# Kernel optimization log

Measured on AMD Instinct MI355X. Metric: run time of the kernel, lower is better.

## Reference

```python
import jax, jax.numpy as jnp
import numpy as np

B, C, H, W = 8, 8, 512, 512

# one-pixel shifts with zero padding (equivalent to the bmm with shift matrices)
def shift_right(x):  # out[..., c] = x[..., c-1]
    return jnp.pad(x, ((0, 0), (0, 0), (1, 0)))[:, :, :-1]
def shift_left(x):   # out[..., c] = x[..., c+1]
    return jnp.pad(x, ((0, 0), (0, 0), (0, 1)))[:, :, 1:]
def shift_up(x):     # out[r] = x[r+1]
    return jnp.pad(x, ((0, 0), (0, 1), (0, 0)))[:, 1:, :]
def shift_down(x):   # out[r] = x[r-1]
    return jnp.pad(x, ((0, 0), (1, 0), (0, 0)))[:, :-1, :]

def bilater_voting(c):
    # c: [B, 8, H, W] probabilities
    right        = shift_right(c[:, 4])
    left         = shift_left(c[:, 3])
    left_bottom  = shift_left(shift_down(c[:, 5]))
    right_above  = shift_right(shift_up(c[:, 2]))
    left_above   = shift_left(shift_up(c[:, 0]))
    bottom       = shift_down(c[:, 6])
    up           = shift_up(c[:, 1])
    right_bottom = shift_right(shift_down(c[:, 7]))
    a1 = c[:, 3] * right
    a2 = c[:, 4] * left
    a3 = c[:, 1] * bottom
    a4 = c[:, 6] * up
    a5 = c[:, 2] * left_bottom
    a6 = c[:, 5] * right_above
    a7 = c[:, 0] * right_bottom
    a8 = c[:, 7] * left_above
    vote_out = jnp.stack([a7, a3, a5, a1, a2, a6, a4, a8], axis=1)
    glo_map = jnp.mean(vote_out, axis=1)
    return glo_map, vote_out

def bce(p, t):
    # matches torch F.binary_cross_entropy (mean reduction, log clamped at -100)
    logp = jnp.clip(jnp.log(p), -100.0, None)
    log1mp = jnp.clip(jnp.log(1.0 - p), -100.0, None)
    return -jnp.mean(t * logp + (1.0 - t) * log1mp)

def setup_inputs() -> dict:
    key = jax.random.key(0)
    k1, k2, k3, k4 = jax.random.split(key, 4)
    atts = jax.random.normal(k1, (B, C, H, W), dtype=jnp.float32)
    dets = jax.random.normal(k2, (B, C, H, W), dtype=jnp.float32)
    target = jax.random.randint(k3, (B, 1, H, W), 0, 2).astype(jnp.float32)
    con_target = jax.random.randint(k4, (B, C, H, W), 0, 2).astype(jnp.float32)
    return {"atts": atts, "dets": dets, "target": target, "con_target": con_target}

def reference(atts, dets, target, con_target):
    # edge mask from connectivity GT: pixels with 0 < sum < 8
    sum_conn = jnp.sum(con_target, axis=1)  # [B, H, W]
    edge_conn = jnp.where((sum_conn < 8.0) & (sum_conn > 0.0), 1.0, 0.0)

    atts_p = jax.nn.sigmoid(atts)
    dets_p = jax.nn.sigmoid(dets)

    glo_map1, vote_out1 = bilater_voting(atts_p)
    glo_map2, vote_out2 = bilater_voting(dets_p)

    # edge/decouple loss on dets branch
    pred_mask_min = 1.0 - jnp.min(vote_out2, axis=1)
    pred_mask_min = pred_mask_min * edge_conn
    decouple_map = glo_map2 * (1.0 - edge_conn) + pred_mask_min
    de_loss2 = bce(decouple_map[:, None], target)

    bce_loss1 = bce(glo_map1[:, None], target)
    bicon_loss1 = bce(vote_out1, con_target)
    conn_loss1 = bce(atts_p, con_target)
    bicon_loss2 = bce(vote_out2, con_target)
    conn_loss2 = bce(dets_p, con_target)

    loss = (0.2 * bicon_loss1 + 0.8 * conn_loss1 + bce_loss1
            + 0.2 * bicon_loss2 + 0.8 * conn_loss2 + de_loss2)
    return loss
```

## Files before the change

kernel.cpp:

```cpp
#include <hip/hip_runtime.h>
#include <stdint.h>

#define BB 8
#define CC 8
#define HH 512
#define WW 512
#define HWSZ (HH * WW)

typedef float v4 __attribute__((ext_vector_type(4)));

#define LOG2_CLAMP -144.26950409f

__device__ __forceinline__ v4 uload4(const float* __restrict__ p) {
    v4 r;
    __builtin_memcpy(&r, p, sizeof(v4));
    return r;
}
__device__ __forceinline__ v4 aload4(const float* __restrict__ p) {
    return *(const v4* __restrict__)p;
}

__device__ __forceinline__ v4 sig4(v4 x) {
    v4 r;
#pragma unroll
    for (int i = 0; i < 4; ++i)
        r[i] = __builtin_amdgcn_rcpf(1.0f + __expf(-x[i]));
    return r;
}

template <bool NEED_MIN>
__device__ __forceinline__ void eval_branch(
    const v4* __restrict__ cr, const v4* __restrict__ nr, uint32_t sel,
    const float* __restrict__ mkA, const float* __restrict__ mkB,
    const float* __restrict__ mkC,
    v4& glo, v4& vmin, float& Lbic, float& Lcon)
{
    const v4 one = {1.f, 1.f, 1.f, 1.f};
    v4 pb0 = one, pb1 = one, pc = one;
    v4 vsum = {0.f, 0.f, 0.f, 0.f};
    if (NEED_MIN) vmin = {1e30f, 1e30f, 1e30f, 1e30f};

#pragma unroll
    for (int k = 0; k < 8; ++k) {
        v4 s = sig4(cr[k]);
        v4 n = sig4(nr[k]);
        n[0] *= mkA[k]; n[1] *= mkB[k]; n[2] *= mkB[k]; n[3] *= mkC[k];
        v4 v = s * n;
        vsum += v;
        if (NEED_MIN) vmin = __builtin_elementwise_min(vmin, v);
        v4 av, as;
#pragma unroll
        for (int i = 0; i < 4; ++i) {
            const bool bt = (sel >> (k * 4 + i)) & 1u;
            av[i] = bt ? v[i] : 1.0f - v[i];
            as[i] = bt ? s[i] : 1.0f - s[i];
        }
        if (k < 4) pb0 *= av; else pb1 *= av;
        pc *= as;
    }
    glo = vsum * 0.125f;

    float lb = 0.f, lc = 0.f;
#pragma unroll
    for (int i = 0; i < 4; ++i) {
        lb += fmaxf(__log2f(pb0[i]), LOG2_CLAMP) + fmaxf(__log2f(pb1[i]), LOG2_CLAMP);
        lc += fmaxf(__log2f(pc[i]), LOG2_CLAMP);
    }
    Lbic = lb;
    Lcon = lc;
}

__global__ __launch_bounds__(256, 2) void bicon_loss_kernel(
    const float* __restrict__ atts, const float* __restrict__ dets,
    const float* __restrict__ target, const float* __restrict__ con,
    float* __restrict__ partial)
{
    const int idx = (int)blockIdx.x * 256 + (int)threadIdx.x;
    const int w0  = (idx & 127) << 2;
    const int row = idx >> 7;
    const int h   = row & (HH - 1);
    const int b   = row >> 9;

    const int hm = (h > 0) ? h - 1 : 0;
    const int hp = (h < HH - 1) ? h + 1 : HH - 1;
    const float mh0 = (h > 0) ? 1.0f : 0.0f;
    const float mh1 = (h < HH - 1) ? 1.0f : 0.0f;
    const float mw0 = (w0 == 0) ? 0.0f : 1.0f;
    const float mw3 = (w0 == WW - 4) ? 0.0f : 1.0f;

    const int offC = h * WW + w0;
    const int offU = hm * WW + w0;
    const int offD = hp * WW + w0;

    const float* __restrict__ ab = atts + b * CC * HWSZ;
    const float* __restrict__ db = dets + b * CC * HWSZ;
    const float* __restrict__ cb = con  + b * CC * HWSZ;

    v4 cvv[8];
#pragma unroll
    for (int c = 0; c < 8; ++c) cvv[c] = aload4(cb + c * HWSZ + offC);
    v4 tv = aload4(target + b * HWSZ + offC);

    v4 ac[8], an[8];
#pragma unroll
    for (int c = 0; c < 8; ++c) ac[c] = aload4(ab + c * HWSZ + offC);
    an[0] = uload4(ab + 7 * HWSZ + offU - 1);
    an[1] = aload4(ab + 6 * HWSZ + offU);
    an[2] = uload4(ab + 5 * HWSZ + offU + 1);
    an[3] = uload4(ab + 4 * HWSZ + offC - 1);
    an[4] = uload4(ab + 3 * HWSZ + offC + 1);
    an[5] = uload4(ab + 2 * HWSZ + offD - 1);
    an[6] = aload4(ab + 1 * HWSZ + offD);
    an[7] = uload4(ab + 0 * HWSZ + offD + 1);

    v4 dc[8], dn[8];
#pragma unroll
    for (int c = 0; c < 8; ++c) dc[c] = aload4(db + c * HWSZ + offC);
    dn[0] = uload4(db + 7 * HWSZ + offU - 1);
    dn[1] = aload4(db + 6 * HWSZ + offU);
    dn[2] = uload4(db + 5 * HWSZ + offU + 1);
    dn[3] = uload4(db + 4 * HWSZ + offC - 1);
    dn[4] = uload4(db + 3 * HWSZ + offC + 1);
    dn[5] = uload4(db + 2 * HWSZ + offD - 1);
    dn[6] = aload4(db + 1 * HWSZ + offD);
    dn[7] = uload4(db + 0 * HWSZ + offD + 1);

    uint32_t sel = 0u;
#pragma unroll
    for (int c = 0; c < 8; ++c)
#pragma unroll
        for (int i = 0; i < 4; ++i)
            if (cvv[c][i] > 0.5f) sel |= (1u << (c * 4 + i));
    uint32_t tb = 0u;
#pragma unroll
    for (int i = 0; i < 4; ++i)
        if (tv[i] > 0.5f) tb |= (1u << i);

    const float mkA[8] = {mh0 * mw0, mh0, mh0,       mw0, 1.f, mh1 * mw0, mh1, mh1};
    const float mkB[8] = {mh0,       mh0, mh0,       1.f, 1.f, mh1,       mh1, mh1};
    const float mkC[8] = {mh0,       mh0, mh0 * mw3, 1.f, mw3, mh1,       mh1, mh1 * mw3};

    v4 glo1, glo2, vmin1, vmin2;
    float Lb1, Lc1, Lb2, Lc2;
    eval_branch<false>(ac, an, sel, mkA, mkB, mkC, glo1, vmin1, Lb1, Lc1);
    eval_branch<true >(dc, dn, sel, mkA, mkB, mkC, glo2, vmin2, Lb2, Lc2);

    float Lp = 0.f;
#pragma unroll
    for (int i = 0; i < 4; ++i) {
        const uint32_t mI    = 0x11111111u << i;
        const uint32_t bitsI = sel & mI;
        const bool edge = (bitsI != 0u) && (bitsI != mI);
        const float dec = edge ? (1.0f - vmin2[i]) : glo2[i];
        const bool  ti  = (tb >> i) & 1u;
        const float a   = ti ? glo1[i] : 1.0f - glo1[i];
        const float bs  = ti ? dec     : 1.0f - dec;
        Lp += fmaxf(__log2f(a * bs), LOG2_CLAMP);
    }

    const float wbic = 0.2f / (float)(BB * CC * HWSZ);
    const float wcon = 0.8f / (float)(BB * CC * HWSZ);
    const float wpix = 1.0f / (float)(BB * HWSZ);
    const float ln2  = 0.69314718056f;

    float local = -(wbic * (Lb1 + Lb2) + wcon * (Lc1 + Lc2) + wpix * Lp) * ln2;

#pragma unroll
    for (int off = 32; off > 0; off >>= 1)
        local += __shfl_down(local, off, 64);

    __shared__ float wsum[4];
    const int lane = threadIdx.x & 63;
    const int wid  = threadIdx.x >> 6;
    if (lane == 0) wsum[wid] = local;
    __syncthreads();
    if (threadIdx.x == 0)
        partial[blockIdx.x] = wsum[0] + wsum[1] + wsum[2] + wsum[3];
}

__global__ __launch_bounds__(256, 1) void reduce_kernel(
    const float* __restrict__ partial, float* __restrict__ out)
{
    const int tid = (int)threadIdx.x;
    float s = 0.f;
#pragma unroll
    for (int i = 0; i < 8; ++i) s += partial[tid + i * 256];
#pragma unroll
    for (int off = 32; off > 0; off >>= 1)
        s += __shfl_down(s, off, 64);
    __shared__ float ws[4];
    if ((tid & 63) == 0) ws[tid >> 6] = s;
    __syncthreads();
    if (tid == 0) out[0] = ws[0] + ws[1] + ws[2] + ws[3];
}

extern "C" void kernel_launch(void* const* d_in, const int* in_sizes, int n_in,
                              void* d_out, int out_size, void* d_ws, size_t ws_size,
                              hipStream_t stream) {
    const float* atts   = (const float*)d_in[0];
    const float* dets   = (const float*)d_in[1];
    const float* target = (const float*)d_in[2];
    const float* con    = (const float*)d_in[3];
    float* out     = (float*)d_out;
    float* partial = (float*)d_ws;

    const int nblocks = BB * HH * WW / 4 / 256;
    bicon_loss_kernel<<<nblocks, 256, 0, stream>>>(atts, dets, target, con, partial);
    reduce_kernel<<<1, 256, 0, stream>>>(partial, out);
}
```

Before: 202.5 us.

## Process two rows per thread and fetch horizontal neighbours via lane shuffles

Each thread now computes two adjacent rows of four pixels, so the vertical neighbour data for the inner rows comes from registers instead of extra global loads. Horizontal one-pixel shifts are built with wave shuffles of the aligned vectors instead of unaligned vector loads. Only the wave-edge lanes fall back to scalar global loads. The aim is to cut redundant and misaligned memory traffic, at the cost of roughly doubling live registers per thread, which risks spills or lower occupancy. The grid is halved and the final reduction is adjusted to match.

```diff
diff --git a/kernel.cpp b/kernel.cpp
--- a/kernel.cpp
+++ b/kernel.cpp
@@ -11,11 +11,6 @@
 
 #define LOG2_CLAMP -144.26950409f
 
-__device__ __forceinline__ v4 uload4(const float* __restrict__ p) {
-    v4 r;
-    __builtin_memcpy(&r, p, sizeof(v4));
-    return r;
-}
 __device__ __forceinline__ v4 aload4(const float* __restrict__ p) {
     return *(const v4* __restrict__)p;
 }
@@ -28,8 +23,15 @@
     return r;
 }
 
+__device__ __forceinline__ void mk_masks(float mh0, float mh1, float mw0, float mw3,
+                                         float* A, float* B, float* C) {
+    A[0]=mh0*mw0; A[1]=mh0; A[2]=mh0;     A[3]=mw0; A[4]=1.f; A[5]=mh1*mw0; A[6]=mh1; A[7]=mh1;
+    B[0]=mh0;     B[1]=mh0; B[2]=mh0;     B[3]=1.f; B[4]=1.f; B[5]=mh1;     B[6]=mh1; B[7]=mh1;
+    C[0]=mh0;     C[1]=mh0; C[2]=mh0*mw3; C[3]=1.f; C[4]=mw3; C[5]=mh1;     C[6]=mh1; C[7]=mh1*mw3;
+}
+
 template <bool NEED_MIN>
-__device__ __forceinline__ void eval_branch(
+__device__ __forceinline__ void eval_row(
     const v4* __restrict__ cr, const v4* __restrict__ nr, uint32_t sel,
     const float* __restrict__ mkA, const float* __restrict__ mkB,
     const float* __restrict__ mkC,
@@ -59,15 +61,75 @@
         pc *= as;
     }
     glo = vsum * 0.125f;
-
-    float lb = 0.f, lc = 0.f;
 #pragma unroll
     for (int i = 0; i < 4; ++i) {
-        lb += fmaxf(__log2f(pb0[i]), LOG2_CLAMP) + fmaxf(__log2f(pb1[i]), LOG2_CLAMP);
-        lc += fmaxf(__log2f(pc[i]), LOG2_CLAMP);
-    }
-    Lbic = lb;
-    Lcon = lc;
+        Lbic += fmaxf(__log2f(pb0[i]), LOG2_CLAMP) + fmaxf(__log2f(pb1[i]), LOG2_CLAMP);
+        Lcon += fmaxf(__log2f(pc[i]), LOG2_CLAMP);
+    }
+}
+
+template <bool NEED_MIN>
+__device__ __forceinline__ void eval_input(
+    const float* __restrict__ Xb,
+    const v4* __restrict__ x0, const v4* __restrict__ x1,
+    v4 xu7, v4 xu6, v4 xu5, v4 xd2, v4 xd1, v4 xd0,
+    int offC0, int offC1, int offU, int offD, int lane,
+    uint32_t sel0, uint32_t sel1,
+    const float* __restrict__ mkA0, const float* __restrict__ mkB0,
+    const float* __restrict__ mkC0,
+    const float* __restrict__ mkA1, const float* __restrict__ mkB1,
+    const float* __restrict__ mkC1,
+    v4& glo0, v4& glo1, v4& vmin0, v4& vmin1, float& Lb, float& Lc)
+{
+    float cm[6] = { __shfl(xu7[3],   lane - 1, 64),
+                    __shfl(x0[4][3], lane - 1, 64),
+                    __shfl(x1[2][3], lane - 1, 64),
+                    __shfl(x0[7][3], lane - 1, 64),
+                    __shfl(x1[4][3], lane - 1, 64),
+                    __shfl(xd2[3],   lane - 1, 64) };
+    if (lane == 0) {
+        cm[0] = Xb[7 * HWSZ + offU  - 1];
+        cm[1] = Xb[4 * HWSZ + offC0 - 1];
+        cm[2] = Xb[2 * HWSZ + offC1 - 1];
+        cm[3] = Xb[7 * HWSZ + offC0 - 1];
+        cm[4] = Xb[4 * HWSZ + offC1 - 1];
+        cm[5] = Xb[2 * HWSZ + offD  - 1];
+    }
+    float cp[6] = { __shfl(xu5[0],   lane + 1, 64),
+                    __shfl(x0[3][0], lane + 1, 64),
+                    __shfl(x1[0][0], lane + 1, 64),
+                    __shfl(x0[5][0], lane + 1, 64),
+                    __shfl(x1[3][0], lane + 1, 64),
+                    __shfl(xd0[0],   lane + 1, 64) };
+    if (lane == 63) {
+        cp[0] = Xb[5 * HWSZ + offU  + 4];
+        cp[1] = Xb[3 * HWSZ + offC0 + 4];
+        cp[2] = Xb[0 * HWSZ + offC1 + 4];
+        cp[3] = Xb[5 * HWSZ + offC0 + 4];
+        cp[4] = Xb[3 * HWSZ + offC1 + 4];
+        cp[5] = Xb[0 * HWSZ + offD  + 4];
+    }
+
+    v4 n[8];
+    n[0] = (v4){cm[0], xu7[0], xu7[1], xu7[2]};
+    n[1] = xu6;
+    n[2] = (v4){xu5[1], xu5[2], xu5[3], cp[0]};
+    n[3] = (v4){cm[1], x0[4][0], x0[4][1], x0[4][2]};
+    n[4] = (v4){x0[3][1], x0[3][2], x0[3][3], cp[1]};
+    n[5] = (v4){cm[2], x1[2][0], x1[2][1], x1[2][2]};
+    n[6] = x1[1];
+    n[7] = (v4){x1[0][1], x1[0][2], x1[0][3], cp[2]};
+    eval_row<NEED_MIN>(x0, n, sel0, mkA0, mkB0, mkC0, glo0, vmin0, Lb, Lc);
+
+    n[0] = (v4){cm[3], x0[7][0], x0[7][1], x0[7][2]};
+    n[1] = x0[6];
+    n[2] = (v4){x0[5][1], x0[5][2], x0[5][3], cp[3]};
+    n[3] = (v4){cm[4], x1[4][0], x1[4][1], x1[4][2]};
+    n[4] = (v4){x1[3][1], x1[3][2], x1[3][3], cp[4]};
+    n[5] = (v4){cm[5], xd2[0], xd2[1], xd2[2]};
+    n[6] = xd1;
+    n[7] = (v4){xd0[1], xd0[2], xd0[3], cp[5]};
+    eval_row<NEED_MIN>(x1, n, sel1, mkA1, mkB1, mkC1, glo1, vmin1, Lb, Lc);
 }
 
 __global__ __launch_bounds__(256, 2) void bicon_loss_kernel(
@@ -75,87 +137,117 @@
     const float* __restrict__ target, const float* __restrict__ con,
     float* __restrict__ partial)
 {
-    const int idx = (int)blockIdx.x * 256 + (int)threadIdx.x;
-    const int w0  = (idx & 127) << 2;
-    const int row = idx >> 7;
-    const int h   = row & (HH - 1);
-    const int b   = row >> 9;
-
-    const int hm = (h > 0) ? h - 1 : 0;
-    const int hp = (h < HH - 1) ? h + 1 : HH - 1;
-    const float mh0 = (h > 0) ? 1.0f : 0.0f;
-    const float mh1 = (h < HH - 1) ? 1.0f : 0.0f;
-    const float mw0 = (w0 == 0) ? 0.0f : 1.0f;
-    const float mw3 = (w0 == WW - 4) ? 0.0f : 1.0f;
-
-    const int offC = h * WW + w0;
-    const int offU = hm * WW + w0;
-    const int offD = hp * WW + w0;
+    const int tid   = (int)threadIdx.x;
+    const int bid   = (int)blockIdx.x;
+    const int b     = bid >> 7;
+    const int br    = bid & 127;
+    const int strip = tid >> 7;
+    const int cg    = tid & 127;
+    const int lane  = tid & 63;
+    const int h     = br * 4 + strip * 2;
+    const int w0    = cg << 2;
+
+    const int hm  = (h > 0) ? h - 1 : 0;
+    const int hp2 = (h + 2 < HH) ? h + 2 : HH - 1;
+
+    const float mw0   = (w0 == 0) ? 0.f : 1.f;
+    const float mw3   = (w0 == WW - 4) ? 0.f : 1.f;
+    const float mh0r0 = (h > 0) ? 1.f : 0.f;
+    const float mh1r1 = (h + 1 < HH - 1) ? 1.f : 0.f;
+
+    const int offC0 = h * WW + w0;
+    const int offC1 = offC0 + WW;
+    const int offU  = hm * WW + w0;
+    const int offD  = hp2 * WW + w0;
 
     const float* __restrict__ ab = atts + b * CC * HWSZ;
     const float* __restrict__ db = dets + b * CC * HWSZ;
     const float* __restrict__ cb = con  + b * CC * HWSZ;
 
-    v4 cvv[8];
-#pragma unroll
-    for (int c = 0; c < 8; ++c) cvv[c] = aload4(cb + c * HWSZ + offC);
-    v4 tv = aload4(target + b * HWSZ + offC);
-
-    v4 ac[8], an[8];
-#pragma unroll
-    for (int c = 0; c < 8; ++c) ac[c] = aload4(ab + c * HWSZ + offC);
-    an[0] = uload4(ab + 7 * HWSZ + offU - 1);
-    an[1] = aload4(ab + 6 * HWSZ + offU);
-    an[2] = uload4(ab + 5 * HWSZ + offU + 1);
-    an[3] = uload4(ab + 4 * HWSZ + offC - 1);
-    an[4] = uload4(ab + 3 * HWSZ + offC + 1);
-    an[5] = uload4(ab + 2 * HWSZ + offD - 1);
-    an[6] = aload4(ab + 1 * HWSZ + offD);
-    an[7] = uload4(ab + 0 * HWSZ + offD + 1);
-
-    v4 dc[8], dn[8];
-#pragma unroll
-    for (int c = 0; c < 8; ++c) dc[c] = aload4(db + c * HWSZ + offC);
-    dn[0] = uload4(db + 7 * HWSZ + offU - 1);
-    dn[1] = aload4(db + 6 * HWSZ + offU);
-    dn[2] = uload4(db + 5 * HWSZ + offU + 1);
-    dn[3] = uload4(db + 4 * HWSZ + offC - 1);
-    dn[4] = uload4(db + 3 * HWSZ + offC + 1);
-    dn[5] = uload4(db + 2 * HWSZ + offD - 1);
-    dn[6] = aload4(db + 1 * HWSZ + offD);
-    dn[7] = uload4(db + 0 * HWSZ + offD + 1);
-
-    uint32_t sel = 0u;
+    v4 cv0[8], cv1[8];
+#pragma unroll
+    for (int c = 0; c < 8; ++c) {
+        cv0[c] = aload4(cb + c * HWSZ + offC0);
+        cv1[c] = aload4(cb + c * HWSZ + offC1);
+    }
+    v4 tv0 = aload4(target + b * HWSZ + offC0);
+    v4 tv1 = aload4(target + b * HWSZ + offC1);
+
+    v4 a0[8], a1[8];
+#pragma unroll
+    for (int c = 0; c < 8; ++c) {
+        a0[c] = aload4(ab + c * HWSZ + offC0);
+        a1[c] = aload4(ab + c * HWSZ + offC1);
+    }
+    v4 au7 = aload4(ab + 7 * HWSZ + offU);
+    v4 au6 = aload4(ab + 6 * HWSZ + offU);
+    v4 au5 = aload4(ab + 5 * HWSZ + offU);
+    v4 ad2 = aload4(ab + 2 * HWSZ + offD);
+    v4 ad1 = aload4(ab + 1 * HWSZ + offD);
+    v4 ad0 = aload4(ab + 0 * HWSZ + offD);
+
+    v4 d0[8], d1[8];
+#pragma unroll
+    for (int c = 0; c < 8; ++c) {
+        d0[c] = aload4(db + c * HWSZ + offC0);
+        d1[c] = aload4(db + c * HWSZ + offC1);
+    }
+    v4 du7 = aload4(db + 7 * HWSZ + offU);
+    v4 du6 = aload4(db + 6 * HWSZ + offU);
+    v4 du5 = aload4(db + 5 * HWSZ + offU);
+    v4 dd2 = aload4(db + 2 * HWSZ + offD);
+    v4 dd1 = aload4(db + 1 * HWSZ + offD);
+    v4 dd0 = aload4(db + 0 * HWSZ + offD);
+
+    uint32_t sel0 = 0u, sel1 = 0u;
 #pragma unroll
     for (int c = 0; c < 8; ++c)
 #pragma unroll
-        for (int i = 0; i < 4; ++i)
-            if (cvv[c][i] > 0.5f) sel |= (1u << (c * 4 + i));
-    uint32_t tb = 0u;
-#pragma unroll
-    for (int i = 0; i < 4; ++i)
-        if (tv[i] > 0.5f) tb |= (1u << i);
-
-    const float mkA[8] = {mh0 * mw0, mh0, mh0,       mw0, 1.f, mh1 * mw0, mh1, mh1};
-    const float mkB[8] = {mh0,       mh0, mh0,       1.f, 1.f, mh1,       mh1, mh1};
-    const float mkC[8] = {mh0,       mh0, mh0 * mw3, 1.f, mw3, mh1,       mh1, mh1 * mw3};
-
-    v4 glo1, glo2, vmin1, vmin2;
-    float Lb1, Lc1, Lb2, Lc2;
-    eval_branch<false>(ac, an, sel, mkA, mkB, mkC, glo1, vmin1, Lb1, Lc1);
-    eval_branch<true >(dc, dn, sel, mkA, mkB, mkC, glo2, vmin2, Lb2, Lc2);
+        for (int i = 0; i < 4; ++i) {
+            if (cv0[c][i] > 0.5f) sel0 |= (1u << (c * 4 + i));
+            if (cv1[c][i] > 0.5f) sel1 |= (1u << (c * 4 + i));
+        }
+    uint32_t tb0 = 0u, tb1 = 0u;
+#pragma unroll
+    for (int i = 0; i < 4; ++i) {
+        if (tv0[i] > 0.5f) tb0 |= (1u << i);
+        if (tv1[i] > 0.5f) tb1 |= (1u << i);
+    }
+
+    float mkA0[8], mkB0[8], mkC0[8], mkA1[8], mkB1[8], mkC1[8];
+    mk_masks(mh0r0, 1.f, mw0, mw3, mkA0, mkB0, mkC0);
+    mk_masks(1.f, mh1r1, mw0, mw3, mkA1, mkB1, mkC1);
+
+    float Lb1 = 0.f, Lc1 = 0.f, Lb2 = 0.f, Lc2 = 0.f;
+    v4 g1r0, g1r1, g2r0, g2r1, vm2r0, vm2r1, vdum0, vdum1;
+    eval_input<false>(ab, a0, a1, au7, au6, au5, ad2, ad1, ad0,
+                      offC0, offC1, offU, offD, lane, sel0, sel1,
+                      mkA0, mkB0, mkC0, mkA1, mkB1, mkC1,
+                      g1r0, g1r1, vdum0, vdum1, Lb1, Lc1);
+    eval_input<true >(db, d0, d1, du7, du6, du5, dd2, dd1, dd0,
+                      offC0, offC1, offU, offD, lane, sel0, sel1,
+                      mkA0, mkB0, mkC0, mkA1, mkB1, mkC1,
+                      g2r0, g2r1, vm2r0, vm2r1, Lb2, Lc2);
 
     float Lp = 0.f;
 #pragma unroll
-    for (int i = 0; i < 4; ++i) {
-        const uint32_t mI    = 0x11111111u << i;
-        const uint32_t bitsI = sel & mI;
-        const bool edge = (bitsI != 0u) && (bitsI != mI);
-        const float dec = edge ? (1.0f - vmin2[i]) : glo2[i];
-        const bool  ti  = (tb >> i) & 1u;
-        const float a   = ti ? glo1[i] : 1.0f - glo1[i];
-        const float bs  = ti ? dec     : 1.0f - dec;
-        Lp += fmaxf(__log2f(a * bs), LOG2_CLAMP);
+    for (int r = 0; r < 2; ++r) {
+        const uint32_t sel = r ? sel1 : sel0;
+        const uint32_t tb  = r ? tb1  : tb0;
+        const v4 g1 = r ? g1r1 : g1r0;
+        const v4 g2 = r ? g2r1 : g2r0;
+        const v4 vm = r ? vm2r1 : vm2r0;
+#pragma unroll
+        for (int i = 0; i < 4; ++i) {
+            const uint32_t mI    = 0x11111111u << i;
+            const uint32_t bitsI = sel & mI;
+            const bool edge = (bitsI != 0u) && (bitsI != mI);
+            const float dec = edge ? (1.0f - vm[i]) : g2[i];
+            const bool  ti  = (tb >> i) & 1u;
+            const float aa  = ti ? g1[i] : 1.0f - g1[i];
+            const float bs  = ti ? dec   : 1.0f - dec;
+            Lp += fmaxf(__log2f(aa * bs), LOG2_CLAMP);
+        }
     }
 
     const float wbic = 0.2f / (float)(BB * CC * HWSZ);
@@ -170,12 +262,11 @@
         local += __shfl_down(local, off, 64);
 
     __shared__ float wsum[4];
-    const int lane = threadIdx.x & 63;
-    const int wid  = threadIdx.x >> 6;
+    const int wid = tid >> 6;
     if (lane == 0) wsum[wid] = local;
     __syncthreads();
-    if (threadIdx.x == 0)
-        partial[blockIdx.x] = wsum[0] + wsum[1] + wsum[2] + wsum[3];
+    if (tid == 0)
+        partial[bid] = wsum[0] + wsum[1] + wsum[2] + wsum[3];
 }
 
 __global__ __launch_bounds__(256, 1) void reduce_kernel(
@@ -184,7 +275,7 @@
     const int tid = (int)threadIdx.x;
     float s = 0.f;
 #pragma unroll
-    for (int i = 0; i < 8; ++i) s += partial[tid + i * 256];
+    for (int i = 0; i < 4; ++i) s += partial[tid + i * 256];
 #pragma unroll
     for (int off = 32; off > 0; off >>= 1)
         s += __shfl_down(s, off, 64);
@@ -204,7 +295,7 @@
     float* out     = (float*)d_out;
     float* partial = (float*)d_ws;
 
-    const int nblocks = BB * HH * WW / 4 / 256;
+    const int nblocks = BB * (HH / 4);
     bicon_loss_kernel<<<nblocks, 256, 0, stream>>>(atts, dets, target, con, partial);
     reduce_kernel<<<1, 256, 0, stream>>>(partial, out);
 }
```

Result: slower. 243.9 us (+20.4%).

## Share stencil neighbors via wave shuffles with 2-row wave tiles

Applied to the files above, without the earlier changes.

Each wavefront now covers two adjacent rows of 128 columns. Vertical neighbors come from the paired half-wave via lane-xor-32 shuffles, and horizontal neighbors from adjacent-lane shuffles. Each thread loads only three aligned halo vectors plus a few scalar edge values, replacing eight unaligned neighbor loads per input. This cuts global load count and unaligned accesses, in exchange for many cross-lane shuffle instructions and extra register pressure.

```diff
diff --git a/kernel.cpp b/kernel.cpp
--- a/kernel.cpp
+++ b/kernel.cpp
@@ -11,11 +11,6 @@
 
 #define LOG2_CLAMP -144.26950409f
 
-__device__ __forceinline__ v4 uload4(const float* __restrict__ p) {
-    v4 r;
-    __builtin_memcpy(&r, p, sizeof(v4));
-    return r;
-}
 __device__ __forceinline__ v4 aload4(const float* __restrict__ p) {
     return *(const v4* __restrict__)p;
 }
@@ -28,11 +23,17 @@
     return r;
 }
 
+__device__ __forceinline__ v4 shflv4(v4 v, int src) {
+    v4 r;
+#pragma unroll
+    for (int i = 0; i < 4; ++i) r[i] = __shfl(v[i], src, 64);
+    return r;
+}
+
 template <bool NEED_MIN>
-__device__ __forceinline__ void eval_branch(
+__device__ __forceinline__ void eval_row(
     const v4* __restrict__ cr, const v4* __restrict__ nr, uint32_t sel,
-    const float* __restrict__ mkA, const float* __restrict__ mkB,
-    const float* __restrict__ mkC,
+    float mh0, float mh1, float mw0, float mw3,
     v4& glo, v4& vmin, float& Lbic, float& Lcon)
 {
     const v4 one = {1.f, 1.f, 1.f, 1.f};
@@ -42,9 +43,12 @@
 
 #pragma unroll
     for (int k = 0; k < 8; ++k) {
+        const float rowm = (k < 3) ? mh0 : ((k >= 5) ? mh1 : 1.f);
+        const float m0 = (k == 0 || k == 3 || k == 5) ? mw0 * rowm : rowm;
+        const float m3 = (k == 2 || k == 4 || k == 7) ? mw3 * rowm : rowm;
         v4 s = sig4(cr[k]);
         v4 n = sig4(nr[k]);
-        n[0] *= mkA[k]; n[1] *= mkB[k]; n[2] *= mkB[k]; n[3] *= mkC[k];
+        n[0] *= m0; n[1] *= rowm; n[2] *= rowm; n[3] *= m3;
         v4 v = s * n;
         vsum += v;
         if (NEED_MIN) vmin = __builtin_elementwise_min(vmin, v);
@@ -59,15 +63,50 @@
         pc *= as;
     }
     glo = vsum * 0.125f;
-
-    float lb = 0.f, lc = 0.f;
 #pragma unroll
     for (int i = 0; i < 4; ++i) {
-        lb += fmaxf(__log2f(pb0[i]), LOG2_CLAMP) + fmaxf(__log2f(pb1[i]), LOG2_CLAMP);
-        lc += fmaxf(__log2f(pc[i]), LOG2_CLAMP);
-    }
-    Lbic = lb;
-    Lcon = lc;
+        Lbic += fmaxf(__log2f(pb0[i]), LOG2_CLAMP) + fmaxf(__log2f(pb1[i]), LOG2_CLAMP);
+        Lcon += fmaxf(__log2f(pc[i]), LOG2_CLAMP);
+    }
+}
+
+template <bool NEED_MIN>
+__device__ __forceinline__ void eval_input(
+    const v4* __restrict__ x, const v4* __restrict__ hq,
+    const float* __restrict__ cL, const float* __restrict__ cR,
+    int lane, int rsel, int cg, uint32_t sel,
+    float mh0, float mh1, float mw0, float mw3,
+    v4& glo, v4& vmin, float& Lb, float& Lc)
+{
+    const int po = lane ^ 32;
+    v4 s7 = shflv4(x[7], po), s6 = shflv4(x[6], po), s5 = shflv4(x[5], po);
+    v4 s2 = shflv4(x[2], po), s1 = shflv4(x[1], po), s0 = shflv4(x[0], po);
+    const v4 up7 = rsel ? s7 : hq[0];
+    const v4 up6 = rsel ? s6 : hq[1];
+    const v4 up5 = rsel ? s5 : hq[2];
+    const v4 dn2 = rsel ? hq[0] : s2;
+    const v4 dn1 = rsel ? hq[1] : s1;
+    const v4 dn0 = rsel ? hq[2] : s0;
+
+    float l0 = __shfl(up7[3],  lane - 1, 64);
+    float l1 = __shfl(x[4][3], lane - 1, 64);
+    float l2 = __shfl(dn2[3],  lane - 1, 64);
+    if (cg == 0) { l0 = cL[0]; l1 = cL[1]; l2 = cL[2]; }
+    float r0 = __shfl(up5[0],  lane + 1, 64);
+    float r1 = __shfl(x[3][0], lane + 1, 64);
+    float r2 = __shfl(dn0[0],  lane + 1, 64);
+    if (cg == 31) { r0 = cR[0]; r1 = cR[1]; r2 = cR[2]; }
+
+    v4 n[8];
+    n[0] = (v4){l0, up7[0], up7[1], up7[2]};
+    n[1] = up6;
+    n[2] = (v4){up5[1], up5[2], up5[3], r0};
+    n[3] = (v4){l1, x[4][0], x[4][1], x[4][2]};
+    n[4] = (v4){x[3][1], x[3][2], x[3][3], r1};
+    n[5] = (v4){l2, dn2[0], dn2[1], dn2[2]};
+    n[6] = dn1;
+    n[7] = (v4){dn0[1], dn0[2], dn0[3], r2};
+    eval_row<NEED_MIN>(x, n, sel, mh0, mh1, mw0, mw3, glo, vmin, Lb, Lc);
 }
 
 __global__ __launch_bounds__(256, 2) void bicon_loss_kernel(
@@ -75,75 +114,101 @@
     const float* __restrict__ target, const float* __restrict__ con,
     float* __restrict__ partial)
 {
-    const int idx = (int)blockIdx.x * 256 + (int)threadIdx.x;
-    const int w0  = (idx & 127) << 2;
-    const int row = idx >> 7;
-    const int h   = row & (HH - 1);
-    const int b   = row >> 9;
-
-    const int hm = (h > 0) ? h - 1 : 0;
-    const int hp = (h < HH - 1) ? h + 1 : HH - 1;
-    const float mh0 = (h > 0) ? 1.0f : 0.0f;
-    const float mh1 = (h < HH - 1) ? 1.0f : 0.0f;
-    const float mw0 = (w0 == 0) ? 0.0f : 1.0f;
-    const float mw3 = (w0 == WW - 4) ? 0.0f : 1.0f;
-
-    const int offC = h * WW + w0;
-    const int offU = hm * WW + w0;
-    const int offD = hp * WW + w0;
+    const int tid  = (int)threadIdx.x;
+    const int bid  = (int)blockIdx.x;
+    const int wave = tid >> 6;
+    const int lane = tid & 63;
+    const int rsel = lane >> 5;
+    const int cg   = lane & 31;
+
+    const int b    = bid >> 8;
+    const int rem  = bid & 255;
+    const int h0   = (rem >> 2) << 3;
+    const int c0   = (rem & 3) << 7;
+
+    const int h  = h0 + (wave << 1) + rsel;
+    const int w0 = c0 + (cg << 2);
+
+    const float mw0 = (w0 == 0) ? 0.f : 1.f;
+    const float mw3 = (w0 == WW - 4) ? 0.f : 1.f;
+    const float mh0 = (h > 0) ? 1.f : 0.f;
+    const float mh1 = (h < HH - 1) ? 1.f : 0.f;
+
+    const int offC  = h * WW + w0;
+    const int hU    = (h > 0) ? h - 1 : 0;
+    const int hD    = (h < HH - 1) ? h + 1 : HH - 1;
+    const int hHalo = rsel ? hD : hU;
+    const int offH  = hHalo * WW + w0;
+    const int colm  = (w0 > 0) ? w0 - 1 : 0;
+    const int colp  = (w0 < WW - 4) ? w0 + 4 : WW - 1;
 
     const float* __restrict__ ab = atts + b * CC * HWSZ;
     const float* __restrict__ db = dets + b * CC * HWSZ;
     const float* __restrict__ cb = con  + b * CC * HWSZ;
 
-    v4 cvv[8];
-#pragma unroll
-    for (int c = 0; c < 8; ++c) cvv[c] = aload4(cb + c * HWSZ + offC);
+    const int hc0 = rsel ? 2 : 7;
+    const int hc1 = rsel ? 1 : 6;
+    const int hc2 = rsel ? 0 : 5;
+
+    v4 cv[8];
+#pragma unroll
+    for (int c = 0; c < 8; ++c) cv[c] = aload4(cb + c * HWSZ + offC);
     v4 tv = aload4(target + b * HWSZ + offC);
 
-    v4 ac[8], an[8];
-#pragma unroll
-    for (int c = 0; c < 8; ++c) ac[c] = aload4(ab + c * HWSZ + offC);
-    an[0] = uload4(ab + 7 * HWSZ + offU - 1);
-    an[1] = aload4(ab + 6 * HWSZ + offU);
-    an[2] = uload4(ab + 5 * HWSZ + offU + 1);
-    an[3] = uload4(ab + 4 * HWSZ + offC - 1);
-    an[4] = uload4(ab + 3 * HWSZ + offC + 1);
-    an[5] = uload4(ab + 2 * HWSZ + offD - 1);
-    an[6] = aload4(ab + 1 * HWSZ + offD);
-    an[7] = uload4(ab + 0 * HWSZ + offD + 1);
-
-    v4 dc[8], dn[8];
-#pragma unroll
-    for (int c = 0; c < 8; ++c) dc[c] = aload4(db + c * HWSZ + offC);
-    dn[0] = uload4(db + 7 * HWSZ + offU - 1);
-    dn[1] = aload4(db + 6 * HWSZ + offU);
-    dn[2] = uload4(db + 5 * HWSZ + offU + 1);
-    dn[3] = uload4(db + 4 * HWSZ + offC - 1);
-    dn[4] = uload4(db + 3 * HWSZ + offC + 1);
-    dn[5] = uload4(db + 2 * HWSZ + offD - 1);
-    dn[6] = aload4(db + 1 * HWSZ + offD);
-    dn[7] = uload4(db + 0 * HWSZ + offD + 1);
+    v4 ax[8], ahq[3];
+#pragma unroll
+    for (int c = 0; c < 8; ++c) ax[c] = aload4(ab + c * HWSZ + offC);
+    ahq[0] = aload4(ab + hc0 * HWSZ + offH);
+    ahq[1] = aload4(ab + hc1 * HWSZ + offH);
+    ahq[2] = aload4(ab + hc2 * HWSZ + offH);
+    float acL[3] = {}, acR[3] = {};
+    if (cg == 0) {
+        acL[0] = ab[7 * HWSZ + hU * WW + colm];
+        acL[1] = ab[4 * HWSZ + h  * WW + colm];
+        acL[2] = ab[2 * HWSZ + hD * WW + colm];
+    }
+    if (cg == 31) {
+        acR[0] = ab[5 * HWSZ + hU * WW + colp];
+        acR[1] = ab[3 * HWSZ + h  * WW + colp];
+        acR[2] = ab[0 * HWSZ + hD * WW + colp];
+    }
 
     uint32_t sel = 0u;
 #pragma unroll
     for (int c = 0; c < 8; ++c)
 #pragma unroll
         for (int i = 0; i < 4; ++i)
-            if (cvv[c][i] > 0.5f) sel |= (1u << (c * 4 + i));
+            if (cv[c][i] > 0.5f) sel |= (1u << (c * 4 + i));
     uint32_t tb = 0u;
 #pragma unroll
     for (int i = 0; i < 4; ++i)
         if (tv[i] > 0.5f) tb |= (1u << i);
 
-    const float mkA[8] = {mh0 * mw0, mh0, mh0,       mw0, 1.f, mh1 * mw0, mh1, mh1};
-    const float mkB[8] = {mh0,       mh0, mh0,       1.f, 1.f, mh1,       mh1, mh1};
-    const float mkC[8] = {mh0,       mh0, mh0 * mw3, 1.f, mw3, mh1,       mh1, mh1 * mw3};
-
-    v4 glo1, glo2, vmin1, vmin2;
-    float Lb1, Lc1, Lb2, Lc2;
-    eval_branch<false>(ac, an, sel, mkA, mkB, mkC, glo1, vmin1, Lb1, Lc1);
-    eval_branch<true >(dc, dn, sel, mkA, mkB, mkC, glo2, vmin2, Lb2, Lc2);
+    v4 dx[8], dhq[3];
+#pragma unroll
+    for (int c = 0; c < 8; ++c) dx[c] = aload4(db + c * HWSZ + offC);
+    dhq[0] = aload4(db + hc0 * HWSZ + offH);
+    dhq[1] = aload4(db + hc1 * HWSZ + offH);
+    dhq[2] = aload4(db + hc2 * HWSZ + offH);
+    float dcL[3] = {}, dcR[3] = {};
+    if (cg == 0) {
+        dcL[0] = db[7 * HWSZ + hU * WW + colm];
+        dcL[1] = db[4 * HWSZ + h  * WW + colm];
+        dcL[2] = db[2 * HWSZ + hD * WW + colm];
+    }
+    if (cg == 31) {
+        dcR[0] = db[5 * HWSZ + hU * WW + colp];
+        dcR[1] = db[3 * HWSZ + h  * WW + colp];
+        dcR[2] = db[0 * HWSZ + hD * WW + colp];
+    }
+
+    float Lb1 = 0.f, Lc1 = 0.f, Lb2 = 0.f, Lc2 = 0.f;
+    v4 glo1, glo2, vmin2, vdum;
+    eval_input<false>(ax, ahq, acL, acR, lane, rsel, cg, sel,
+                      mh0, mh1, mw0, mw3, glo1, vdum, Lb1, Lc1);
+
+    eval_input<true >(dx, dhq, dcL, dcR, lane, rsel, cg, sel,
+                      mh0, mh1, mw0, mw3, glo2, vmin2, Lb2, Lc2);
 
     float Lp = 0.f;
 #pragma unroll
@@ -153,9 +218,9 @@
         const bool edge = (bitsI != 0u) && (bitsI != mI);
         const float dec = edge ? (1.0f - vmin2[i]) : glo2[i];
         const bool  ti  = (tb >> i) & 1u;
-        const float a   = ti ? glo1[i] : 1.0f - glo1[i];
+        const float aa  = ti ? glo1[i] : 1.0f - glo1[i];
         const float bs  = ti ? dec     : 1.0f - dec;
-        Lp += fmaxf(__log2f(a * bs), LOG2_CLAMP);
+        Lp += fmaxf(__log2f(aa * bs), LOG2_CLAMP);
     }
 
     const float wbic = 0.2f / (float)(BB * CC * HWSZ);
@@ -170,12 +235,10 @@
         local += __shfl_down(local, off, 64);
 
     __shared__ float wsum[4];
-    const int lane = threadIdx.x & 63;
-    const int wid  = threadIdx.x >> 6;
-    if (lane == 0) wsum[wid] = local;
+    if (lane == 0) wsum[tid >> 6] = local;
     __syncthreads();
-    if (threadIdx.x == 0)
-        partial[blockIdx.x] = wsum[0] + wsum[1] + wsum[2] + wsum[3];
+    if (tid == 0)
+        partial[bid] = wsum[0] + wsum[1] + wsum[2] + wsum[3];
 }
 
 __global__ __launch_bounds__(256, 1) void reduce_kernel(
@@ -204,7 +267,7 @@
     float* out     = (float*)d_out;
     float* partial = (float*)d_ws;
 
-    const int nblocks = BB * HH * WW / 4 / 256;
+    const int nblocks = BB * (HH / 8) * (WW / 128);
     bicon_loss_kernel<<<nblocks, 256, 0, stream>>>(atts, dets, target, con, partial);
     reduce_kernel<<<1, 256, 0, stream>>>(partial, out);
 }
```

New measurement: 202.7 us. About the same (+0.1%).
